# Kernel tuning notes

Hardware: AMD Instinct MI355X
Metric: run time of the kernel (lower is better)

The kernel has to match this reference:

```python
import jax, jax.numpy as jnp
import numpy as np

HID = 1024
NH = 16
DH = HID // NH  # 64


def _heads(x):
    # [B, S, H] -> [B, nH, S, dh]
    B, S, _ = x.shape
    return x.reshape(B, S, NH, DH).transpose(0, 2, 1, 3)


def setup_inputs() -> dict:
    key = jax.random.key(0)
    ks = jax.random.split(key, 16)
    inp = {
        "word_hidden_states": jax.random.normal(ks[0], (2, 2048, HID), jnp.float32),
        "entity_hidden_states": jax.random.normal(ks[1], (2, 256, HID), jnp.float32),
    }
    scale = 1.0 / np.sqrt(HID)
    names = ["Wq", "Wk", "Wv", "Ww2e", "We2w", "We2e"]
    for i, n in enumerate(names):
        inp[n] = jax.random.normal(ks[2 + i], (HID, HID), jnp.float32) * scale
        inp["b" + n[1:]] = jnp.zeros((HID,), jnp.float32)
    return inp


def reference(word_hidden_states, entity_hidden_states,
              Wq, bq, Wk, bk, Wv, bv,
              Ww2e, bw2e, We2w, be2w, We2e, be2e):
    word, ent = word_hidden_states, entity_hidden_states
    B, Sw, _ = word.shape
    Se = ent.shape[1]
    hs = jnp.concatenate([word, ent], axis=1)  # [B, Sw+Se, H]

    # four query types, heads: [B, nH, S*, dh]
    q_w2w = _heads(word @ Wq + bq)
    q_w2e = _heads(word @ Ww2e + bw2e)
    q_e2w = _heads(ent @ We2w + be2w)
    q_e2e = _heads(ent @ We2e + be2e)

    k = _heads(hs @ Wk + bk)
    v = _heads(hs @ Wv + bv)
    k_w, k_e = k[:, :, :Sw, :], k[:, :, Sw:, :]

    # block scores
    s_w2w = jnp.einsum("bhqd,bhkd->bhqk", q_w2w, k_w)  # [B,nH,Sw,Sw]
    s_w2e = jnp.einsum("bhqd,bhkd->bhqk", q_w2e, k_e)  # [B,nH,Sw,Se]
    s_e2w = jnp.einsum("bhqd,bhkd->bhqk", q_e2w, k_w)  # [B,nH,Se,Sw]
    s_e2e = jnp.einsum("bhqd,bhkd->bhqk", q_e2e, k_e)  # [B,nH,Se,Se]

    word_scores = jnp.concatenate([s_w2w, s_w2e], axis=3)
    ent_scores = jnp.concatenate([s_e2w, s_e2e], axis=3)
    scores = jnp.concatenate([word_scores, ent_scores], axis=2)  # [B,nH,S,S]
    scores = scores / np.sqrt(DH)

    probs = jax.nn.softmax(scores, axis=-1)  # dropout is identity in eval
    ctx = jnp.einsum("bhqk,bhkd->bhqd", probs, v)  # [B,nH,S,dh]
    ctx = ctx.transpose(0, 2, 1, 3).reshape(B, Sw + Se, HID)
    return ctx[:, :Sw, :], ctx[:, Sw:, :]
```

## Files before the change

kernel.cpp:

```cpp
#include <hip/hip_runtime.h>
#include <hip/hip_bf16.h>

typedef __attribute__((ext_vector_type(8))) short short8;
typedef __attribute__((ext_vector_type(4))) float f32x4;
typedef __attribute__((ext_vector_type(16))) float f32x16;
typedef __attribute__((ext_vector_type(4))) unsigned short u16x4;
typedef __attribute__((ext_vector_type(8))) unsigned short u16x8;
typedef __attribute__((ext_vector_type(4))) unsigned int u32x4;

__device__ __forceinline__ unsigned short f2b(float f) {
  __hip_bfloat16 h = __float2bfloat16(f);
  return __builtin_bit_cast(unsigned short, h);
}

__device__ __forceinline__ void gload_lds16(const void* g, void* l) {
  __builtin_amdgcn_global_load_lds(
      (const __attribute__((address_space(1))) unsigned int*)g,
      (__attribute__((address_space(3))) unsigned int*)l, 16, 0, 0);
}

__device__ __forceinline__ f32x16 mfma32(short8 a, short8 b, f32x16 c) {
  return __builtin_amdgcn_mfma_f32_32x32x16_bf16(a, b, c, 0, 0, 0);
}

__device__ __forceinline__ unsigned int cvtpk(float a, float b) {
  unsigned int r;
  asm("v_cvt_pk_bf16_f32 %0, %1, %2" : "=v"(r) : "v"(a), "v"(b));
  return r;
}

__global__ __launch_bounds__(256) void cvt_all(const float* __restrict__ sw,
                                               const float* __restrict__ se,
                                               unsigned short* __restrict__ dw,
                                               unsigned short* __restrict__ de) {
  int i = blockIdx.x * 256 + threadIdx.x;
  const float* s;
  unsigned short* d;
  int j;
  if (i < 524288) {
    s = sw; d = dw; j = i;
  } else {
    s = se; d = de; j = i - 524288;
    if (j >= 65536) return;
  }
  const f32x4* sp = (const f32x4*)s;
  f32x4 a = sp[2 * j];
  f32x4 b = sp[2 * j + 1];
  u16x8 o;
  o[0] = f2b(a[0]); o[1] = f2b(a[1]); o[2] = f2b(a[2]); o[3] = f2b(a[3]);
  o[4] = f2b(b[0]); o[5] = f2b(b[1]); o[6] = f2b(b[2]); o[7] = f2b(b[3]);
  ((u16x8*)d)[j] = o;
}

struct WtransParams {
  const float* w[6];
  unsigned short* wt[6];
};

__global__ __launch_bounds__(256) void wtrans(WtransParams p) {
  __shared__ float t[32][33];
  const int z = blockIdx.z;
  const float* W = p.w[z];
  unsigned short* Wt = p.wt[z];
  const int bx = blockIdx.x;
  const int by = blockIdx.y;
  const int tx = threadIdx.x, ty = threadIdx.y;
#pragma unroll
  for (int i = 0; i < 4; ++i)
    t[ty + 8 * i][tx] = W[(by * 32 + ty + 8 * i) * 1024 + bx * 32 + tx];
  __syncthreads();
#pragma unroll
  for (int i = 0; i < 4; ++i)
    Wt[(bx * 32 + ty + 8 * i) * 1024 + by * 32 + tx] = f2b(t[tx][ty + 8 * i]);
}

struct GemmJob {
  const unsigned short* Wt;
  const float* bias;
  unsigned short* out;
  int S;
  int s_off;
  int sshift;
  int trans;
  float scale;
};
struct Gemm2Params {
  const unsigned short* Aw;
  const unsigned short* Ae;
  GemmJob job[8];
};

__global__ __launch_bounds__(256) void gemm_qkv(Gemm2Params p) {
  __shared__ unsigned short As[128 * 64];
  __shared__ unsigned short Bs[128 * 64];
  const int tid = threadIdx.x;
  const int w = tid >> 6, lane = tid & 63;
  const int c = lane & 15, g = lane >> 4;
  const int z = blockIdx.z;
  const int y = blockIdx.y;
  const bool isw = y < 32;
  const GemmJob j = p.job[isw ? z : z + 4];
  const unsigned short* A = isw ? p.Aw : p.Ae;
  const long arow0 = (long)(isw ? y : y - 32) * 128;
  const unsigned short* B = j.Wt;
  const long brow0 = (long)blockIdx.x * 128;

  f32x4 acc[4][4] = {};

  for (int kt = 0; kt < 16; ++kt) {
    __syncthreads();
#pragma unroll
    for (int i = 0; i < 4; ++i) {
      int ch = i * 256 + tid;
      int row = ch >> 3;
      int k8 = ((ch & 7) ^ (row & 7)) << 3;
      const unsigned short* ga = A + (arow0 + row) * 1024 + kt * 64 + k8;
      const unsigned short* gb = B + (brow0 + row) * 1024 + kt * 64 + k8;
      gload_lds16(ga, As + (i * 256 + w * 64) * 8);
      gload_lds16(gb, Bs + (i * 256 + w * 64) * 8);
    }
    __syncthreads();
#pragma unroll
    for (int kf = 0; kf < 2; ++kf) {
      short8 av[4], bv[4];
#pragma unroll
      for (int mf = 0; mf < 4; ++mf) {
        int row = (w >> 1) * 64 + mf * 16 + c;
        int byte = (row * 128 + (kf * 32 + g * 8) * 2) ^ ((row & 7) << 4);
        av[mf] = *(const short8*)((const char*)As + byte);
      }
#pragma unroll
      for (int nf = 0; nf < 4; ++nf) {
        int row = (w & 1) * 64 + nf * 16 + c;
        int byte = (row * 128 + (kf * 32 + g * 8) * 2) ^ ((row & 7) << 4);
        bv[nf] = *(const short8*)((const char*)Bs + byte);
      }
      __builtin_amdgcn_s_setprio(1);
#pragma unroll
      for (int mf = 0; mf < 4; ++mf)
#pragma unroll
        for (int nf = 0; nf < 4; ++nf)
          acc[mf][nf] = __builtin_amdgcn_mfma_f32_16x16x32_bf16(av[mf], bv[nf],
                                                                acc[mf][nf], 0, 0, 0);
      __builtin_amdgcn_s_setprio(0);
    }
  }

  float biasv[4];
#pragma unroll
  for (int nf = 0; nf < 4; ++nf) {
    int n = (int)brow0 + (w & 1) * 64 + nf * 16 + c;
    biasv[nf] = j.bias[n];
  }
  const int smask = (1 << j.sshift) - 1;
  if (j.trans) {
#pragma unroll
    for (int mf = 0; mf < 4; ++mf) {
      int m0 = (int)arow0 + (w >> 1) * 64 + mf * 16 + g * 4;
      int b_ = m0 >> j.sshift;
      int s = (m0 & smask) + j.s_off;
#pragma unroll
      for (int nf = 0; nf < 4; ++nf) {
        int n = (int)brow0 + (w & 1) * 64 + nf * 16 + c;
        int hh = n >> 6, dd = n & 63;
        u16x4 pv;
#pragma unroll
        for (int r = 0; r < 4; ++r)
          pv[r] = f2b((acc[mf][nf][r] + biasv[nf]) * j.scale);
        *(u16x4*)(j.out + (((long)b_ * 16 + hh) * 64 + dd) * 2304 + s) = pv;
      }
    }
  } else {
#pragma unroll
    for (int mf = 0; mf < 4; ++mf) {
#pragma unroll
      for (int r = 0; r < 4; ++r) {
        int m = (int)arow0 + (w >> 1) * 64 + mf * 16 + g * 4 + r;
        int b_ = m >> j.sshift;
        int s = (m & smask) + j.s_off;
#pragma unroll
        for (int nf = 0; nf < 4; ++nf) {
          int n = (int)brow0 + (w & 1) * 64 + nf * 16 + c;
          int hh = n >> 6, dd = n & 63;
          float v = (acc[mf][nf][r] + biasv[nf]) * j.scale;
          j.out[(((long)b_ * 16 + hh) * j.S + s) * 64 + dd] = f2b(v);
        }
      }
    }
  }
}

__global__ __launch_bounds__(128, 2) void attn_kernel(
    const unsigned short* __restrict__ qw2w, const unsigned short* __restrict__ qw2e,
    const unsigned short* __restrict__ qe2w, const unsigned short* __restrict__ qe2e,
    const unsigned short* __restrict__ Kg, const unsigned short* __restrict__ Vtg,
    float* __restrict__ po0, float* __restrict__ po1, float* __restrict__ lbuf) {
  __shared__ unsigned short smem[16384];

  const int tid = threadIdx.x;
  const int w = tid >> 6, lane = tid & 63;
  const int l31 = lane & 31, hf = lane >> 5;

  const int flat = blockIdx.x;
  const int work = (flat & 7) * 144 + (flat >> 3);
  const int part = work & 1;
  const int tile = (work % 36) >> 1;
  const int hb = work / 36;
  const int head = hb & 15, b = hb >> 4;

  const bool isw = tile < 16;
  const int Sq = isw ? 2048 : 256;
  const int q0 = (isw ? tile : tile - 16) * 128 + w * 64;
  const int bh = b * 16 + head;
  const unsigned short* Qa =
      (isw ? qw2w : qe2w) + ((long)bh * Sq + q0 + l31) * 64 + hf * 8;
  const unsigned short* Qb =
      (isw ? qw2e : qe2e) + ((long)bh * Sq + q0 + l31) * 64 + hf * 8;
  const unsigned short* Kb = Kg + (long)bh * 2304 * 64;
  const unsigned short* Vtb = Vtg + (long)bh * 64 * 2304;

  short8 qcur[2][4];
#pragma unroll
  for (int qh = 0; qh < 2; ++qh)
#pragma unroll
    for (int kf = 0; kf < 4; ++kf)
      qcur[qh][kf] = *(const short8*)(Qa + qh * 32 * 64 + kf * 16);

  f32x16 o[2][2] = {};
  float lrun[2] = {0.f, 0.f};

  auto stage = [&](int t, int bufi) {
    const unsigned short* Kt = Kb + t * 4096;
    unsigned short* Klp = smem + bufi * 4096;
    unsigned short* Vlp = smem + 8192 + bufi * 4096;
#pragma unroll
    for (int i = 0; i < 4; ++i) {
      int ch = i * 128 + tid;
      int row = ch >> 3, c8 = ch & 7;
      int col = (c8 ^ (row & 7)) << 3;
      gload_lds16(Kt + row * 64 + col, Klp + (i * 128 + (tid & 64)) * 8);
      gload_lds16(Vtb + row * 2304 + t * 64 + col, Vlp + (i * 128 + (tid & 64)) * 8);
    }
  };

  const int t0 = part * 18, t1 = t0 + 18;
  stage(t0, 0);
  __syncthreads();
  int cur = 0;

  for (int t = t0; t < t1; ++t) {
    if (t == 32) {
#pragma unroll
      for (int qh = 0; qh < 2; ++qh)
#pragma unroll
        for (int kf = 0; kf < 4; ++kf)
          qcur[qh][kf] = *(const short8*)(Qb + qh * 32 * 64 + kf * 16);
    }
    if (t + 1 < t1) stage(t + 1, cur ^ 1);

    const char* Kbase = (const char*)(smem + cur * 4096);
    const char* Vbase = (const char*)(smem + 8192 + cur * 4096);

#pragma unroll
    for (int kg = 0; kg < 2; ++kg) {
      int row = kg * 32 + l31;
      int rb = (row * 128) | (hf * 16);
      int sw = (row & 7) << 4;
      short8 kfr[4];
#pragma unroll
      for (int kf = 0; kf < 4; ++kf)
        kfr[kf] = *(const short8*)(Kbase + ((rb + kf * 32) ^ sw));
      f32x16 st0 = {}, st1 = {};
      __builtin_amdgcn_s_setprio(1);
#pragma unroll
      for (int kf = 0; kf < 4; ++kf) {
        st0 = mfma32(kfr[kf], qcur[0][kf], st0);
        st1 = mfma32(kfr[kf], qcur[1][kf], st1);
      }
      __builtin_amdgcn_s_setprio(0);

      float s0 = 0.f, s1 = 0.f, s2 = 0.f, s3 = 0.f;
      float u0 = 0.f, u1 = 0.f, u2 = 0.f, u3 = 0.f;
#pragma unroll
      for (int r = 0; r < 16; r += 4) {
        float p0 = __builtin_amdgcn_exp2f(st0[r + 0]);
        float p1 = __builtin_amdgcn_exp2f(st0[r + 1]);
        float p2 = __builtin_amdgcn_exp2f(st0[r + 2]);
        float p3 = __builtin_amdgcn_exp2f(st0[r + 3]);
        st0[r + 0] = p0; st0[r + 1] = p1; st0[r + 2] = p2; st0[r + 3] = p3;
        s0 += p0; s1 += p1; s2 += p2; s3 += p3;
        float q0_ = __builtin_amdgcn_exp2f(st1[r + 0]);
        float q1_ = __builtin_amdgcn_exp2f(st1[r + 1]);
        float q2_ = __builtin_amdgcn_exp2f(st1[r + 2]);
        float q3_ = __builtin_amdgcn_exp2f(st1[r + 3]);
        st1[r + 0] = q0_; st1[r + 1] = q1_; st1[r + 2] = q2_; st1[r + 3] = q3_;
        u0 += q0_; u1 += q1_; u2 += q2_; u3 += q3_;
      }
      lrun[0] += (s0 + s1) + (s2 + s3);
      lrun[1] += (u0 + u1) + (u2 + u3);

#pragma unroll
      for (int hs = 0; hs < 2; ++hs) {
        const int rbase = hs * 8;
        unsigned int a0 = cvtpk(st0[rbase + 0], st0[rbase + 1]);
        unsigned int a1 = cvtpk(st0[rbase + 2], st0[rbase + 3]);
        unsigned int b0 = cvtpk(st0[rbase + 4], st0[rbase + 5]);
        unsigned int b1 = cvtpk(st0[rbase + 6], st0[rbase + 7]);
        asm("v_permlane32_swap_b32 %0, %1" : "+v"(a0), "+v"(b0));
        asm("v_permlane32_swap_b32 %0, %1" : "+v"(a1), "+v"(b1));
        u32x4 pw0;
        pw0[0] = a0; pw0[1] = a1; pw0[2] = b0; pw0[3] = b1;
        short8 pf0 = __builtin_bit_cast(short8, pw0);
        unsigned int c0 = cvtpk(st1[rbase + 0], st1[rbase + 1]);
        unsigned int c1 = cvtpk(st1[rbase + 2], st1[rbase + 3]);
        unsigned int d0 = cvtpk(st1[rbase + 4], st1[rbase + 5]);
        unsigned int d1 = cvtpk(st1[rbase + 6], st1[rbase + 7]);
        asm("v_permlane32_swap_b32 %0, %1" : "+v"(c0), "+v"(d0));
        asm("v_permlane32_swap_b32 %0, %1" : "+v"(c1), "+v"(d1));
        u32x4 pw1;
        pw1[0] = c0; pw1[1] = c1; pw1[2] = d0; pw1[3] = d1;
        short8 pf1 = __builtin_bit_cast(short8, pw1);
        const int ks = kg * 2 + hs;
        short8 vf0, vf1;
        {
          int vrow = l31;
          int byte = ((vrow * 128) | (ks * 32 + hf * 16)) ^ ((vrow & 7) << 4);
          vf0 = *(const short8*)(Vbase + byte);
          vrow = 32 + l31;
          byte = ((vrow * 128) | (ks * 32 + hf * 16)) ^ ((vrow & 7) << 4);
          vf1 = *(const short8*)(Vbase + byte);
        }
        __builtin_amdgcn_s_setprio(1);
        o[0][0] = mfma32(vf0, pf0, o[0][0]);
        o[0][1] = mfma32(vf1, pf0, o[0][1]);
        o[1][0] = mfma32(vf0, pf1, o[1][0]);
        o[1][1] = mfma32(vf1, pf1, o[1][1]);
        __builtin_amdgcn_s_setprio(0);
      }
    }

    __syncthreads();
    cur ^= 1;
  }

  float lt0 = lrun[0] + __shfl_xor(lrun[0], 32);
  float lt1 = lrun[1] + __shfl_xor(lrun[1], 32);

  const int sgb = (isw ? 0 : 2048) + q0;
  if (hf == 0) {
    lbuf[(long)part * 73728 + bh * 2304 + sgb + l31] = lt0;
    lbuf[(long)part * 73728 + bh * 2304 + sgb + 32 + l31] = lt1;
  }

  float* po = part ? po1 : po0;
  float* ob = isw ? po + (((long)b * 2048 + q0) * 1024 + head * 64)
                  : po + (long)2 * 2048 * 1024 +
                        (((long)b * 256 + q0) * 1024 + head * 64);

  float* E = (float*)smem + w * 1024;
#pragma unroll
  for (int qh = 0; qh < 2; ++qh) {
#pragma unroll
    for (int p = 0; p < 2; ++p) {
#pragma unroll
      for (int rg = 0; rg < 4; ++rg) {
        int off = rg * 8 + hf * 4;
        f32x4 v;
        v[0] = o[qh][p][rg * 4 + 0];
        v[1] = o[qh][p][rg * 4 + 1];
        v[2] = o[qh][p][rg * 4 + 2];
        v[3] = o[qh][p][rg * 4 + 3];
        *(f32x4*)(E + l31 * 32 + (off ^ ((l31 & 7) << 2))) = v;
      }
      asm volatile("s_waitcnt lgkmcnt(0)" ::: "memory");
      __builtin_amdgcn_sched_barrier(0);
#pragma unroll
      for (int i = 0; i < 4; ++i) {
        int qr = i * 8 + (lane >> 3);
        int cc = (lane & 7) * 4;
        f32x4 v = *(const f32x4*)(E + qr * 32 + (cc ^ ((qr & 7) << 2)));
        *(f32x4*)(ob + (long)(qh * 32 + qr) * 1024 + p * 32 + cc) = v;
      }
      asm volatile("s_waitcnt lgkmcnt(0)" ::: "memory");
      __builtin_amdgcn_sched_barrier(0);
    }
  }
}

__global__ __launch_bounds__(256) void attn_merge(const float* __restrict__ po0,
                                                  const float* __restrict__ po1,
                                                  const float* __restrict__ lbuf,
                                                  float* __restrict__ out) {
  long i = ((long)blockIdx.x * 256 + threadIdx.x) * 4;
  if (i >= 4718592) return;
  int bh, sg;
  if (i < 4194304) {
    int b = (int)(i >> 21), s = (int)((i >> 10) & 2047), h = (int)((i >> 6) & 15);
    bh = b * 16 + h;
    sg = s;
  } else {
    long j = i - 4194304;
    int b = (int)(j >> 18), s = (int)((j >> 10) & 255), h = (int)((j >> 6) & 15);
    bh = b * 16 + h;
    sg = 2048 + s;
  }
  float l0 = lbuf[bh * 2304 + sg];
  float l1 = lbuf[73728 + bh * 2304 + sg];
  f32x4 a = *(const f32x4*)(po0 + i);
  f32x4 c = *(const f32x4*)(po1 + i);
  float inv = 1.f / (l0 + l1);
  f32x4 r = (a + c) * inv;
  *(f32x4*)(out + i) = r;
}

extern "C" void kernel_launch(void* const* d_in, const int* in_sizes, int n_in,
                              void* d_out, int out_size, void* d_ws, size_t ws_size,
                              hipStream_t stream) {
  (void)in_sizes; (void)n_in; (void)out_size; (void)ws_size;
  const float* word = (const float*)d_in[0];
  const float* ent = (const float*)d_in[1];

  char* ws = (char*)d_ws;
  size_t off = 0;
  auto alloc = [&](size_t bytes) {
    void* p = ws + off;
    off += (bytes + 255) & ~(size_t)255;
    return p;
  };
  unsigned short* Xw = (unsigned short*)alloc(4096ull * 1024 * 2);
  unsigned short* Xe = (unsigned short*)alloc(512ull * 1024 * 2);
  unsigned short* Wt[6];
  for (int i = 0; i < 6; ++i) Wt[i] = (unsigned short*)alloc(1024ull * 1024 * 2);
  unsigned short* qw2w = (unsigned short*)alloc(2ull * 16 * 2048 * 64 * 2);
  unsigned short* qw2e = (unsigned short*)alloc(2ull * 16 * 2048 * 64 * 2);
  unsigned short* qe2w = (unsigned short*)alloc(2ull * 16 * 256 * 64 * 2);
  unsigned short* qe2e = (unsigned short*)alloc(2ull * 16 * 256 * 64 * 2);
  unsigned short* Kbuf = (unsigned short*)alloc(2ull * 16 * 2304 * 64 * 2);
  unsigned short* Vtbuf = (unsigned short*)alloc(2ull * 16 * 64 * 2304 * 2);
  float* po1 = (float*)alloc(4718592ull * 4);
  float* lbuf = (float*)alloc(2ull * 73728 * 4);
  float* po0 = (float*)ws;

  cvt_all<<<2304, 256, 0, stream>>>(word, ent, Xw, Xe);

  WtransParams wp;
  wp.w[0] = (const float*)d_in[2];
  wp.w[1] = (const float*)d_in[4];
  wp.w[2] = (const float*)d_in[6];
  wp.w[3] = (const float*)d_in[8];
  wp.w[4] = (const float*)d_in[10];
  wp.w[5] = (const float*)d_in[12];
  for (int i = 0; i < 6; ++i) wp.wt[i] = Wt[i];
  wtrans<<<dim3(32, 32, 6), dim3(32, 8), 0, stream>>>(wp);

  const float* bq = (const float*)d_in[3];
  const float* bk = (const float*)d_in[5];
  const float* bv = (const float*)d_in[7];
  const float* bw2e = (const float*)d_in[9];
  const float* be2w = (const float*)d_in[11];
  const float* be2e = (const float*)d_in[13];
  const float qs = 0.125f * 1.44269504f;

  Gemm2Params gp;
  gp.Aw = Xw;
  gp.Ae = Xe;
  gp.job[0] = {Wt[0], bq, qw2w, 2048, 0, 11, 0, qs};
  gp.job[1] = {Wt[3], bw2e, qw2e, 2048, 0, 11, 0, qs};
  gp.job[2] = {Wt[1], bk, Kbuf, 2304, 0, 11, 0, 1.f};
  gp.job[3] = {Wt[2], bv, Vtbuf, 2304, 0, 11, 1, 1.f};
  gp.job[4] = {Wt[4], be2w, qe2w, 256, 0, 8, 0, qs};
  gp.job[5] = {Wt[5], be2e, qe2e, 256, 0, 8, 0, qs};
  gp.job[6] = {Wt[1], bk, Kbuf, 2304, 2048, 8, 0, 1.f};
  gp.job[7] = {Wt[2], bv, Vtbuf, 2304, 2048, 8, 1, 1.f};
  gemm_qkv<<<dim3(8, 36, 4), 256, 0, stream>>>(gp);

  attn_kernel<<<1152, 128, 0, stream>>>(qw2w, qw2e, qe2w, qe2e, Kbuf, Vtbuf,
                                        po0, po1, lbuf);
  attn_merge<<<4608, 256, 0, stream>>>(po0, po1, lbuf, (float*)d_out);
}
```

Measured before the change: 154.9 us.

## Split keys across four waves per block and merge partials in LDS

The attention kernel now gives each block a 64-query tile with 256 threads. Each of the four waves handles a quarter of the key range, using its own double-buffered K/V staging and waitcnt-only synchronisation, so block-wide barriers are gone from the loop. The four partial outputs and row sums are reduced in shared memory at the end and written normalized straight to the output. This removes the separate merge kernel and the round trip of fp32 partial buffers through global memory. The cost is more LDS per block (about 65 KB), which may limit occupancy, and each wave now issues smaller per-tile loads.

Result: faster. 149.1 us (-3.8%).

```diff
diff --git a/kernel.cpp b/kernel.cpp
--- a/kernel.cpp
+++ b/kernel.cpp
@@ -190,12 +190,12 @@
   }
 }
 
-__global__ __launch_bounds__(128, 2) void attn_kernel(
+__global__ __launch_bounds__(256, 2) void attn_kernel(
     const unsigned short* __restrict__ qw2w, const unsigned short* __restrict__ qw2e,
     const unsigned short* __restrict__ qe2w, const unsigned short* __restrict__ qe2e,
     const unsigned short* __restrict__ Kg, const unsigned short* __restrict__ Vtg,
-    float* __restrict__ po0, float* __restrict__ po1, float* __restrict__ lbuf) {
-  __shared__ unsigned short smem[16384];
+    float* __restrict__ out) {
+  __shared__ unsigned short smem[33280];
 
   const int tid = threadIdx.x;
   const int w = tid >> 6, lane = tid & 63;
@@ -203,14 +203,13 @@
 
   const int flat = blockIdx.x;
   const int work = (flat & 7) * 144 + (flat >> 3);
-  const int part = work & 1;
-  const int tile = (work % 36) >> 1;
+  const int tile = work % 36;
   const int hb = work / 36;
   const int head = hb & 15, b = hb >> 4;
 
-  const bool isw = tile < 16;
+  const bool isw = tile < 32;
   const int Sq = isw ? 2048 : 256;
-  const int q0 = (isw ? tile : tile - 16) * 128 + w * 64;
+  const int q0 = (isw ? tile : tile - 32) * 64;
   const int bh = b * 16 + head;
   const unsigned short* Qa =
       (isw ? qw2w : qe2w) + ((long)bh * Sq + q0 + l31) * 64 + hf * 8;
@@ -224,193 +223,160 @@
   for (int qh = 0; qh < 2; ++qh)
 #pragma unroll
     for (int kf = 0; kf < 4; ++kf)
-      qcur[qh][kf] = *(const short8*)(Qa + qh * 32 * 64 + kf * 16);
+      qcur[qh][kf] = *(const short8*)(Qa + qh * 2048 + kf * 16);
 
   f32x16 o[2][2] = {};
   float lrun[2] = {0.f, 0.f};
 
   auto stage = [&](int t, int bufi) {
-    const unsigned short* Kt = Kb + t * 4096;
-    unsigned short* Klp = smem + bufi * 4096;
-    unsigned short* Vlp = smem + 8192 + bufi * 4096;
+    unsigned short* kb = smem + w * 8192 + bufi * 4096;
+    unsigned short* vb = kb + 2048;
+    const int key0s = w * 576 + t * 32;
 #pragma unroll
     for (int i = 0; i < 4; ++i) {
-      int ch = i * 128 + tid;
-      int row = ch >> 3, c8 = ch & 7;
-      int col = (c8 ^ (row & 7)) << 3;
-      gload_lds16(Kt + row * 64 + col, Klp + (i * 128 + (tid & 64)) * 8);
-      gload_lds16(Vtb + row * 2304 + t * 64 + col, Vlp + (i * 128 + (tid & 64)) * 8);
+      int c = i * 64 + lane;
+      int row = c >> 3, slot = c & 7;
+      int sl = slot ^ (row & 7);
+      gload_lds16(Kb + (key0s + row) * 64 + sl * 8, kb + i * 512);
+      int d = row + ((sl >> 2) << 5);
+      int k8 = (sl & 3) << 3;
+      gload_lds16(Vtb + (long)d * 2304 + key0s + k8, vb + i * 512);
     }
   };
 
-  const int t0 = part * 18, t1 = t0 + 18;
-  stage(t0, 0);
-  __syncthreads();
+  stage(0, 0);
   int cur = 0;
-
-  for (int t = t0; t < t1; ++t) {
-    if (t == 32) {
+  const int swz = (l31 & 7) << 4;
+
+  for (int t = 0; t < 18; ++t) {
+    if (w * 576 + t * 32 == 2048) {
 #pragma unroll
       for (int qh = 0; qh < 2; ++qh)
 #pragma unroll
         for (int kf = 0; kf < 4; ++kf)
-          qcur[qh][kf] = *(const short8*)(Qb + qh * 32 * 64 + kf * 16);
-    }
-    if (t + 1 < t1) stage(t + 1, cur ^ 1);
-
-    const char* Kbase = (const char*)(smem + cur * 4096);
-    const char* Vbase = (const char*)(smem + 8192 + cur * 4096);
-
-#pragma unroll
-    for (int kg = 0; kg < 2; ++kg) {
-      int row = kg * 32 + l31;
-      int rb = (row * 128) | (hf * 16);
-      int sw = (row & 7) << 4;
-      short8 kfr[4];
-#pragma unroll
-      for (int kf = 0; kf < 4; ++kf)
-        kfr[kf] = *(const short8*)(Kbase + ((rb + kf * 32) ^ sw));
-      f32x16 st0 = {}, st1 = {};
+          qcur[qh][kf] = *(const short8*)(Qb + qh * 2048 + kf * 16);
+    }
+    if (t < 17) {
+      stage(t + 1, cur ^ 1);
+      asm volatile("s_waitcnt vmcnt(8)" ::: "memory");
+    } else {
+      asm volatile("s_waitcnt vmcnt(0)" ::: "memory");
+    }
+    __builtin_amdgcn_sched_barrier(0);
+
+    const char* KbaseC = (const char*)(smem + w * 8192 + cur * 4096);
+    const char* VbaseC = KbaseC + 4096;
+
+    short8 kfr[4];
+#pragma unroll
+    for (int kf = 0; kf < 4; ++kf)
+      kfr[kf] = *(const short8*)(KbaseC + l31 * 128 + (((kf * 32) | (hf * 16)) ^ swz));
+    f32x16 st0 = {}, st1 = {};
+    __builtin_amdgcn_s_setprio(1);
+#pragma unroll
+    for (int kf = 0; kf < 4; ++kf) {
+      st0 = mfma32(kfr[kf], qcur[0][kf], st0);
+      st1 = mfma32(kfr[kf], qcur[1][kf], st1);
+    }
+    __builtin_amdgcn_s_setprio(0);
+
+    float s0 = 0.f, s1 = 0.f, s2 = 0.f, s3 = 0.f;
+    float u0 = 0.f, u1 = 0.f, u2 = 0.f, u3 = 0.f;
+#pragma unroll
+    for (int r = 0; r < 16; r += 4) {
+      float p0 = __builtin_amdgcn_exp2f(st0[r + 0]);
+      float p1 = __builtin_amdgcn_exp2f(st0[r + 1]);
+      float p2 = __builtin_amdgcn_exp2f(st0[r + 2]);
+      float p3 = __builtin_amdgcn_exp2f(st0[r + 3]);
+      st0[r + 0] = p0; st0[r + 1] = p1; st0[r + 2] = p2; st0[r + 3] = p3;
+      s0 += p0; s1 += p1; s2 += p2; s3 += p3;
+      float q0_ = __builtin_amdgcn_exp2f(st1[r + 0]);
+      float q1_ = __builtin_amdgcn_exp2f(st1[r + 1]);
+      float q2_ = __builtin_amdgcn_exp2f(st1[r + 2]);
+      float q3_ = __builtin_amdgcn_exp2f(st1[r + 3]);
+      st1[r + 0] = q0_; st1[r + 1] = q1_; st1[r + 2] = q2_; st1[r + 3] = q3_;
+      u0 += q0_; u1 += q1_; u2 += q2_; u3 += q3_;
+    }
+    lrun[0] += (s0 + s1) + (s2 + s3);
+    lrun[1] += (u0 + u1) + (u2 + u3);
+
+#pragma unroll
+    for (int hs = 0; hs < 2; ++hs) {
+      const int rbase = hs * 8;
+      unsigned int a0 = cvtpk(st0[rbase + 0], st0[rbase + 1]);
+      unsigned int a1 = cvtpk(st0[rbase + 2], st0[rbase + 3]);
+      unsigned int b0 = cvtpk(st0[rbase + 4], st0[rbase + 5]);
+      unsigned int b1 = cvtpk(st0[rbase + 6], st0[rbase + 7]);
+      asm("v_permlane32_swap_b32 %0, %1" : "+v"(a0), "+v"(b0));
+      asm("v_permlane32_swap_b32 %0, %1" : "+v"(a1), "+v"(b1));
+      u32x4 pw0;
+      pw0[0] = a0; pw0[1] = a1; pw0[2] = b0; pw0[3] = b1;
+      short8 pf0 = __builtin_bit_cast(short8, pw0);
+      unsigned int c0 = cvtpk(st1[rbase + 0], st1[rbase + 1]);
+      unsigned int c1 = cvtpk(st1[rbase + 2], st1[rbase + 3]);
+      unsigned int d0 = cvtpk(st1[rbase + 4], st1[rbase + 5]);
+      unsigned int d1 = cvtpk(st1[rbase + 6], st1[rbase + 7]);
+      asm("v_permlane32_swap_b32 %0, %1" : "+v"(c0), "+v"(d0));
+      asm("v_permlane32_swap_b32 %0, %1" : "+v"(c1), "+v"(d1));
+      u32x4 pw1;
+      pw1[0] = c0; pw1[1] = c1; pw1[2] = d0; pw1[3] = d1;
+      short8 pf1 = __builtin_bit_cast(short8, pw1);
+      short8 vf0 = *(const short8*)(VbaseC + l31 * 128 +
+                                    (((hs * 2 + hf) ^ (l31 & 7)) << 4));
+      short8 vf1 = *(const short8*)(VbaseC + l31 * 128 +
+                                    (((4 + hs * 2 + hf) ^ (l31 & 7)) << 4));
       __builtin_amdgcn_s_setprio(1);
-#pragma unroll
-      for (int kf = 0; kf < 4; ++kf) {
-        st0 = mfma32(kfr[kf], qcur[0][kf], st0);
-        st1 = mfma32(kfr[kf], qcur[1][kf], st1);
-      }
+      o[0][0] = mfma32(vf0, pf0, o[0][0]);
+      o[0][1] = mfma32(vf1, pf0, o[0][1]);
+      o[1][0] = mfma32(vf0, pf1, o[1][0]);
+      o[1][1] = mfma32(vf1, pf1, o[1][1]);
       __builtin_amdgcn_s_setprio(0);
-
-      float s0 = 0.f, s1 = 0.f, s2 = 0.f, s3 = 0.f;
-      float u0 = 0.f, u1 = 0.f, u2 = 0.f, u3 = 0.f;
-#pragma unroll
-      for (int r = 0; r < 16; r += 4) {
-        float p0 = __builtin_amdgcn_exp2f(st0[r + 0]);
-        float p1 = __builtin_amdgcn_exp2f(st0[r + 1]);
-        float p2 = __builtin_amdgcn_exp2f(st0[r + 2]);
-        float p3 = __builtin_amdgcn_exp2f(st0[r + 3]);
-        st0[r + 0] = p0; st0[r + 1] = p1; st0[r + 2] = p2; st0[r + 3] = p3;
-        s0 += p0; s1 += p1; s2 += p2; s3 += p3;
-        float q0_ = __builtin_amdgcn_exp2f(st1[r + 0]);
-        float q1_ = __builtin_amdgcn_exp2f(st1[r + 1]);
-        float q2_ = __builtin_amdgcn_exp2f(st1[r + 2]);
-        float q3_ = __builtin_amdgcn_exp2f(st1[r + 3]);
-        st1[r + 0] = q0_; st1[r + 1] = q1_; st1[r + 2] = q2_; st1[r + 3] = q3_;
-        u0 += q0_; u1 += q1_; u2 += q2_; u3 += q3_;
-      }
-      lrun[0] += (s0 + s1) + (s2 + s3);
-      lrun[1] += (u0 + u1) + (u2 + u3);
-
-#pragma unroll
-      for (int hs = 0; hs < 2; ++hs) {
-        const int rbase = hs * 8;
-        unsigned int a0 = cvtpk(st0[rbase + 0], st0[rbase + 1]);
-        unsigned int a1 = cvtpk(st0[rbase + 2], st0[rbase + 3]);
-        unsigned int b0 = cvtpk(st0[rbase + 4], st0[rbase + 5]);
-        unsigned int b1 = cvtpk(st0[rbase + 6], st0[rbase + 7]);
-        asm("v_permlane32_swap_b32 %0, %1" : "+v"(a0), "+v"(b0));
-        asm("v_permlane32_swap_b32 %0, %1" : "+v"(a1), "+v"(b1));
-        u32x4 pw0;
-        pw0[0] = a0; pw0[1] = a1; pw0[2] = b0; pw0[3] = b1;
-        short8 pf0 = __builtin_bit_cast(short8, pw0);
-        unsigned int c0 = cvtpk(st1[rbase + 0], st1[rbase + 1]);
-        unsigned int c1 = cvtpk(st1[rbase + 2], st1[rbase + 3]);
-        unsigned int d0 = cvtpk(st1[rbase + 4], st1[rbase + 5]);
-        unsigned int d1 = cvtpk(st1[rbase + 6], st1[rbase + 7]);
-        asm("v_permlane32_swap_b32 %0, %1" : "+v"(c0), "+v"(d0));
-        asm("v_permlane32_swap_b32 %0, %1" : "+v"(c1), "+v"(d1));
-        u32x4 pw1;
-        pw1[0] = c0; pw1[1] = c1; pw1[2] = d0; pw1[3] = d1;
-        short8 pf1 = __builtin_bit_cast(short8, pw1);
-        const int ks = kg * 2 + hs;
-        short8 vf0, vf1;
-        {
-          int vrow = l31;
-          int byte = ((vrow * 128) | (ks * 32 + hf * 16)) ^ ((vrow & 7) << 4);
-          vf0 = *(const short8*)(Vbase + byte);
-          vrow = 32 + l31;
-          byte = ((vrow * 128) | (ks * 32 + hf * 16)) ^ ((vrow & 7) << 4);
-          vf1 = *(const short8*)(Vbase + byte);
-        }
-        __builtin_amdgcn_s_setprio(1);
-        o[0][0] = mfma32(vf0, pf0, o[0][0]);
-        o[0][1] = mfma32(vf1, pf0, o[0][1]);
-        o[1][0] = mfma32(vf0, pf1, o[1][0]);
-        o[1][1] = mfma32(vf1, pf1, o[1][1]);
-        __builtin_amdgcn_s_setprio(0);
-      }
-    }
-
-    __syncthreads();
+    }
+
     cur ^= 1;
   }
 
   float lt0 = lrun[0] + __shfl_xor(lrun[0], 32);
   float lt1 = lrun[1] + __shfl_xor(lrun[1], 32);
-
-  const int sgb = (isw ? 0 : 2048) + q0;
-  if (hf == 0) {
-    lbuf[(long)part * 73728 + bh * 2304 + sgb + l31] = lt0;
-    lbuf[(long)part * 73728 + bh * 2304 + sgb + 32 + l31] = lt1;
-  }
-
-  float* po = part ? po1 : po0;
-  float* ob = isw ? po + (((long)b * 2048 + q0) * 1024 + head * 64)
-                  : po + (long)2 * 2048 * 1024 +
-                        (((long)b * 256 + q0) * 1024 + head * 64);
-
-  float* E = (float*)smem + w * 1024;
-#pragma unroll
-  for (int qh = 0; qh < 2; ++qh) {
-#pragma unroll
-    for (int p = 0; p < 2; ++p) {
+  float* Lf = (float*)(smem + 32768);
+  if (lane < 32) {
+    Lf[w * 64 + lane] = lt0;
+    Lf[w * 64 + 32 + lane] = lt1;
+  }
+#pragma unroll
+  for (int qh = 0; qh < 2; ++qh)
+#pragma unroll
+    for (int mf = 0; mf < 2; ++mf)
 #pragma unroll
       for (int rg = 0; rg < 4; ++rg) {
-        int off = rg * 8 + hf * 4;
+        int q = qh * 32 + l31;
+        int d4 = mf * 8 + rg * 2 + hf;
         f32x4 v;
-        v[0] = o[qh][p][rg * 4 + 0];
-        v[1] = o[qh][p][rg * 4 + 1];
-        v[2] = o[qh][p][rg * 4 + 2];
-        v[3] = o[qh][p][rg * 4 + 3];
-        *(f32x4*)(E + l31 * 32 + (off ^ ((l31 & 7) << 2))) = v;
+        v[0] = o[qh][mf][rg * 4 + 0];
+        v[1] = o[qh][mf][rg * 4 + 1];
+        v[2] = o[qh][mf][rg * 4 + 2];
+        v[3] = o[qh][mf][rg * 4 + 3];
+        *(f32x4*)((char*)smem + w * 16384 + q * 256 + ((d4 ^ (q & 7)) << 4)) = v;
       }
-      asm volatile("s_waitcnt lgkmcnt(0)" ::: "memory");
-      __builtin_amdgcn_sched_barrier(0);
-#pragma unroll
-      for (int i = 0; i < 4; ++i) {
-        int qr = i * 8 + (lane >> 3);
-        int cc = (lane & 7) * 4;
-        f32x4 v = *(const f32x4*)(E + qr * 32 + (cc ^ ((qr & 7) << 2)));
-        *(f32x4*)(ob + (long)(qh * 32 + qr) * 1024 + p * 32 + cc) = v;
-      }
-      asm volatile("s_waitcnt lgkmcnt(0)" ::: "memory");
-      __builtin_amdgcn_sched_barrier(0);
-    }
-  }
-}
-
-__global__ __launch_bounds__(256) void attn_merge(const float* __restrict__ po0,
-                                                  const float* __restrict__ po1,
-                                                  const float* __restrict__ lbuf,
-                                                  float* __restrict__ out) {
-  long i = ((long)blockIdx.x * 256 + threadIdx.x) * 4;
-  if (i >= 4718592) return;
-  int bh, sg;
-  if (i < 4194304) {
-    int b = (int)(i >> 21), s = (int)((i >> 10) & 2047), h = (int)((i >> 6) & 15);
-    bh = b * 16 + h;
-    sg = s;
-  } else {
-    long j = i - 4194304;
-    int b = (int)(j >> 18), s = (int)((j >> 10) & 255), h = (int)((j >> 6) & 15);
-    bh = b * 16 + h;
-    sg = 2048 + s;
-  }
-  float l0 = lbuf[bh * 2304 + sg];
-  float l1 = lbuf[73728 + bh * 2304 + sg];
-  f32x4 a = *(const f32x4*)(po0 + i);
-  f32x4 c = *(const f32x4*)(po1 + i);
-  float inv = 1.f / (l0 + l1);
-  f32x4 r = (a + c) * inv;
-  *(f32x4*)(out + i) = r;
+  __syncthreads();
+
+  float* ob = isw ? out + (((long)b * 2048 + q0) * 1024 + head * 64)
+                  : out + 4194304 + (((long)b * 256 + q0) * 1024 + head * 64);
+  const int q = tid >> 2;
+  float inv = 1.f / (Lf[q] + Lf[64 + q] + Lf[128 + q] + Lf[192 + q]);
+#pragma unroll
+  for (int i = 0; i < 4; ++i) {
+    int c = (tid & 3) * 4 + i;
+    f32x4 s = {};
+#pragma unroll
+    for (int ww = 0; ww < 4; ++ww) {
+      f32x4 pv = *(const f32x4*)((const char*)smem + ww * 16384 + q * 256 +
+                                 ((c ^ (q & 7)) << 4));
+      s += pv;
+    }
+    s *= inv;
+    *(f32x4*)(ob + (long)q * 1024 + c * 4) = s;
+  }
 }
 
 extern "C" void kernel_launch(void* const* d_in, const int* in_sizes, int n_in,
@@ -437,9 +403,6 @@
   unsigned short* qe2e = (unsigned short*)alloc(2ull * 16 * 256 * 64 * 2);
   unsigned short* Kbuf = (unsigned short*)alloc(2ull * 16 * 2304 * 64 * 2);
   unsigned short* Vtbuf = (unsigned short*)alloc(2ull * 16 * 64 * 2304 * 2);
-  float* po1 = (float*)alloc(4718592ull * 4);
-  float* lbuf = (float*)alloc(2ull * 73728 * 4);
-  float* po0 = (float*)ws;
 
   cvt_all<<<2304, 256, 0, stream>>>(word, ent, Xw, Xe);
 
@@ -474,7 +437,6 @@
   gp.job[7] = {Wt[2], bv, Vtbuf, 2304, 2048, 8, 1, 1.f};
   gemm_qkv<<<dim3(8, 36, 4), 256, 0, stream>>>(gp);
 
-  attn_kernel<<<1152, 128, 0, stream>>>(qw2w, qw2e, qe2w, qe2e, Kbuf, Vtbuf,
-                                        po0, po1, lbuf);
-  attn_merge<<<4608, 256, 0, stream>>>(po0, po1, lbuf, (float*)d_out);
-}
+  attn_kernel<<<1152, 256, 0, stream>>>(qw2w, qw2e, qe2w, qe2e, Kbuf, Vtbuf,
+                                        (float*)d_out);
+}
```
